# Performance work log

Measured on AMD Instinct MI355X. Metric: run time of the kernel, lower is better.

Reference implementation:

```python
import jax, jax.numpy as jnp
import numpy as np

N, E, C = 50000, 600000, 128
BN_EPS = 1e-5
NORM_EPS = 1e-12


def _edgeconv(x, src, dst, wa, ba, g, be, rm, rv, wb, bb):
    # PyG EdgeConv: message = MLP(concat(x_i, x_j - x_i)); aggr='add' at target i
    x_i = x[dst]                      # [E, C] target features
    x_j = x[src]                      # [E, C] source features
    m = jnp.concatenate([x_i, x_j - x_i], axis=-1)   # [E, 2C]
    m = jax.nn.relu(m @ wa.T + ba)                   # Linear(2C->C) + ReLU
    m = (m - rm) * (g * jax.lax.rsqrt(rv + BN_EPS)) + be  # BatchNorm1d (eval)
    m = m @ wb.T + bb                                # Linear(C->C)
    return jax.ops.segment_sum(m, dst, num_segments=x.shape[0])  # [N, C]


def _lin(k, fan_in, shape):
    bound = 1.0 / np.sqrt(fan_in)
    return jax.random.uniform(k, shape, jnp.float32, -bound, bound)


def setup_inputs() -> dict:
    key = jax.random.key(0)
    ks = jax.random.split(key, 16)
    inp = {
        "x": jax.random.normal(ks[0], (N, C), jnp.float32),
        "edge_index": jax.random.randint(ks[1], (2, E), 0, N, jnp.int64),
    }
    # layer 1 params
    inp["w1a"] = _lin(ks[2], 2 * C, (C, 2 * C)); inp["b1a"] = _lin(ks[3], 2 * C, (C,))
    inp["g1"] = jnp.ones((C,), jnp.float32) + 0.1 * jax.random.normal(ks[4], (C,))
    inp["be1"] = 0.1 * jax.random.normal(ks[5], (C,))
    inp["rm1"] = 0.1 * jax.random.normal(ks[6], (C,))
    inp["rv1"] = 0.5 + jax.random.uniform(ks[7], (C,))
    inp["w1b"] = _lin(ks[8], C, (C, C)); inp["b1b"] = _lin(ks[9], C, (C,))
    # layer 2 params
    inp["w2a"] = _lin(ks[10], 2 * C, (C, 2 * C)); inp["b2a"] = _lin(ks[11], 2 * C, (C,))
    inp["g2"] = jnp.ones((C,), jnp.float32) + 0.1 * jax.random.normal(ks[12], (C,))
    inp["be2"] = 0.1 * jax.random.normal(ks[13], (C,))
    inp["rm2"] = 0.1 * jax.random.normal(ks[14], (C,))
    inp["rv2"] = 0.5 + jax.random.uniform(ks[15], (C,))
    k2 = jax.random.split(ks[15], 2)
    inp["w2b"] = _lin(k2[0], C, (C, C)); inp["b2b"] = _lin(k2[1], C, (C,))
    return inp


def reference(x, edge_index, w1a, b1a, g1, be1, rm1, rv1, w1b, b1b,
              w2a, b2a, g2, be2, rm2, rv2, w2b, b2b):
    src, dst = edge_index[0], edge_index[1]
    # layer 1 (all but last): conv -> relu -> L2 normalize -> dropout(eval=identity)
    h = _edgeconv(x, src, dst, w1a, b1a, g1, be1, rm1, rv1, w1b, b1b)
    h = jax.nn.relu(h)
    h = h / jnp.maximum(jnp.linalg.norm(h, axis=-1, keepdims=True), NORM_EPS)
    # last layer: conv only
    return _edgeconv(h, src, dst, w2a, b2a, g2, be2, rm2, rv2, w2b, b2b)
```

## Files before the change

kernel.cpp:

```cpp
#include <hip/hip_runtime.h>

#define CCH 128
#define WPAD 136
typedef unsigned short ushort;
typedef __attribute__((ext_vector_type(8))) short bf16x8_t;
typedef __attribute__((ext_vector_type(4))) float f32x4;

union ABu { bf16x8_t v; ushort u[8]; uint4 q; };

__device__ __forceinline__ ushort f2b(float f) {
  union { float f; unsigned u; } v{f};
  unsigned r = v.u + 0x7fffu + ((v.u >> 16) & 1u);
  return (ushort)(r >> 16);
}
__device__ __forceinline__ float b2f(ushort s) {
  union { unsigned u; float f; } v{(unsigned)s << 16};
  return v.f;
}

__global__ __launch_bounds__(256) void k_pre(const float* __restrict__ w1a,
                                             const float* __restrict__ w1b,
                                             const float* __restrict__ w2a,
                                             const float* __restrict__ w2b,
                                             ushort* __restrict__ Wcat1, ushort* __restrict__ Wb1,
                                             ushort* __restrict__ Wcat2, ushort* __restrict__ Wb2,
                                             const void* __restrict__ ei, int* __restrict__ deg,
                                             int E) {
  const int b = blockIdx.x, t = threadIdx.x;
  if (b < 128) {
    int i = b * 256 + t;
    int c = i >> 7, k = i & 127;
    float v = (c < 128) ? w1a[c * 256 + k] - w1a[c * 256 + 128 + k]
                        : w1a[(c - 128) * 256 + 128 + k];
    Wcat1[i] = f2b(v);
    if (i < 16384) Wb1[i] = f2b(w1b[i]);
  } else if (b < 256) {
    int i = (b - 128) * 256 + t;
    int c = i >> 7, k = i & 127;
    float v = (c < 128) ? w2a[c * 256 + k] - w2a[c * 256 + 128 + k]
                        : w2a[(c - 128) * 256 + 128 + k];
    Wcat2[i] = f2b(v);
    if (i < 16384) Wb2[i] = f2b(w2b[i]);
  } else {
    __shared__ int nz;
    if (t == 0) nz = 0;
    __syncthreads();
    int e = (b - 256) * 256 + t;
    unsigned hi = (e < E) ? ((const unsigned*)ei)[2 * (size_t)e + 1] : 0u;
    if (hi) atomicAdd(&nz, 1);
    __syncthreads();
    bool i64 = (nz == 0);
    if (e < E) {
      int d = i64 ? (int)((const long long*)ei)[(size_t)E + e]
                  : ((const int*)ei)[(size_t)E + e];
      atomicAdd(&deg[d], 1);
    }
  }
}

__global__ __launch_bounds__(256) void k_rowptr(const int* __restrict__ deg,
                                                const int* __restrict__ bsum,
                                                int* __restrict__ rowptr,
                                                int n, int nb, int Etot) {
  __shared__ int s[256];
  const int t = threadIdx.x, b = blockIdx.x;
  s[t] = (t < nb && t < b) ? bsum[t] : 0;
  __syncthreads();
  for (int off = 128; off > 0; off >>= 1) {
    if (t < off) s[t] += s[t + off];
    __syncthreads();
  }
  int boffset = s[0];
  __syncthreads();
  int i = b * 256 + t;
  int v = (i < n) ? deg[i] : 0;
  s[t] = v; __syncthreads();
  for (int off = 1; off < 256; off <<= 1) {
    int tv = (t >= off) ? s[t - off] : 0;
    __syncthreads();
    s[t] += tv;
    __syncthreads();
  }
  if (i < n) rowptr[i] = boffset + s[t] - v;
  if (b == gridDim.x - 1 && t == 0) rowptr[n] = Etot;
}

__global__ __launch_bounds__(256) void k_scatter(const void* __restrict__ ei,
                                                 const int* __restrict__ rowptr,
                                                 int* __restrict__ cnt,
                                                 int* __restrict__ esrc, int E) {
  __shared__ int nz;
  const int t = threadIdx.x;
  if (t == 0) nz = 0;
  __syncthreads();
  int e = blockIdx.x * 256 + t;
  unsigned hi = (e < E) ? ((const unsigned*)ei)[2 * (size_t)e + 1] : 0u;
  if (hi) atomicAdd(&nz, 1);
  __syncthreads();
  bool i64 = (nz == 0);
  if (e < E) {
    int d, sv;
    if (i64) {
      sv = (int)((const long long*)ei)[(size_t)e];
      d  = (int)((const long long*)ei)[(size_t)E + e];
    } else {
      sv = ((const int*)ei)[(size_t)e];
      d  = ((const int*)ei)[(size_t)E + e];
    }
    int pos = rowptr[d] + atomicAdd(&cnt[d], 1);
    esrc[pos] = sv;
  }
}

__device__ __forceinline__ void stage_w(const ushort* __restrict__ Wp,
                                        ushort* __restrict__ wlds, int t) {
  for (int i = t; i < 128 * 16; i += 256) {
    int row = i >> 4, ch = i & 15;
    *(uint4*)&wlds[row * WPAD + ch * 8] = *(const uint4*)&Wp[row * CCH + ch * 8];
  }
}

__device__ __forceinline__ void load_a1_bf16(const ushort* __restrict__ XB,
                                             int ar, int quad, int nN, ABu a[4]) {
#pragma unroll
  for (int kk = 0; kk < 4; ++kk)
    a[kk].q = (ar < nN) ? *(const uint4*)(XB + (size_t)ar * CCH + kk * 32 + quad * 8)
                        : make_uint4(0, 0, 0, 0);
}

__device__ __forceinline__ void load_a1_f32(const float* __restrict__ X,
                                            int ar, int quad, int nN, ABu a[4]) {
#pragma unroll
  for (int kk = 0; kk < 4; ++kk) {
    if (ar < nN) {
      const float* p = X + (size_t)ar * CCH + kk * 32 + quad * 8;
      float4 f0 = *(const float4*)p, f1 = *(const float4*)(p + 4);
      a[kk].u[0] = f2b(f0.x); a[kk].u[1] = f2b(f0.y);
      a[kk].u[2] = f2b(f0.z); a[kk].u[3] = f2b(f0.w);
      a[kk].u[4] = f2b(f1.x); a[kk].u[5] = f2b(f1.y);
      a[kk].u[6] = f2b(f1.z); a[kk].u[7] = f2b(f1.w);
    } else a[kk].q = make_uint4(0, 0, 0, 0);
  }
}

__device__ __forceinline__ void load_a1_lds(const ushort* __restrict__ hlds,
                                            int lr, int quad, ABu a[4]) {
#pragma unroll
  for (int kk = 0; kk < 4; ++kk)
    a[kk].q = *(const uint4*)&hlds[lr * WPAD + kk * 32 + quad * 8];
}

__device__ __forceinline__ void mma1(const ABu a[4],
                                     const ushort* __restrict__ wlds,
                                     int ln, int quad, f32x4 acc[8]) {
#pragma unroll
  for (int s = 0; s < 8; ++s) acc[s] = (f32x4){0.f, 0.f, 0.f, 0.f};
#pragma unroll
  for (int s = 0; s < 8; ++s) {
#pragma unroll
    for (int kk = 0; kk < 4; ++kk) {
      ABu b;
      b.q = *(const uint4*)&wlds[(s * 16 + ln) * WPAD + kk * 32 + quad * 8];
      acc[s] = __builtin_amdgcn_mfma_f32_16x16x32_bf16(a[kk].v, b.v, acc[s], 0, 0, 0);
    }
  }
}

__device__ __forceinline__ void epi1(f32x4 acc[8], int rowb, int ln, int quad, int nN,
                                     const float* bias, int half, ushort* dst) {
#pragma unroll
  for (int s = 0; s < 8; ++s) {
    int col = s * 16 + ln;
    float bv = half ? 0.f : bias[col];
#pragma unroll
    for (int r = 0; r < 4; ++r) {
      int row = rowb + quad * 4 + r;
      if (row < nN) dst[(size_t)row * CCH + col] = f2b(acc[s][r] + bv);
    }
  }
}

__global__ __launch_bounds__(256) void k_mix1(const float* __restrict__ x,
                                              const ushort* __restrict__ Wcat,
                                              const float* __restrict__ bias,
                                              ushort* __restrict__ A1,
                                              ushort* __restrict__ A2, int nN,
                                              const int* __restrict__ deg,
                                              int* __restrict__ bsum, int gG, int n) {
  __shared__ ushort wlds[128 * WPAD];
  const int t = threadIdx.x;
  if ((int)blockIdx.x >= gG) {
    int* s = (int*)wlds;
    int bb = blockIdx.x - gG;
    int i = bb * 256 + t;
    s[t] = (i < n) ? deg[i] : 0;
    __syncthreads();
    for (int off = 128; off > 0; off >>= 1) {
      if (t < off) s[t] += s[t + off];
      __syncthreads();
    }
    if (t == 0) bsum[bb] = s[0];
    return;
  }
  const int wave = t >> 6, lane = t & 63;
  const int ln = lane & 15, quad = lane >> 4;
  const int rowb = blockIdx.x * 64 + wave * 16;
  stage_w(Wcat, wlds, t);
  ABu a[4];
  load_a1_f32(x, rowb + ln, quad, nN, a);
  __syncthreads();
  f32x4 acc[8];
  mma1(a, wlds, ln, quad, acc);
  epi1(acc, rowb, ln, quad, nN, bias, 0, A1);
  __syncthreads();
  stage_w(Wcat + 128 * CCH, wlds, t);
  __syncthreads();
  mma1(a, wlds, ln, quad, acc);
  epi1(acc, rowb, ln, quad, nN, bias, 1, A2);
}

__global__ __launch_bounds__(256) void k_fuse12(const ushort* __restrict__ MB,
                                                const ushort* __restrict__ Wb1,
                                                const float* __restrict__ b1b,
                                                const ushort* __restrict__ Wcat2,
                                                const float* __restrict__ b2a,
                                                const int* __restrict__ deg,
                                                ushort* __restrict__ B0,
                                                ushort* __restrict__ B1, int nN) {
  __shared__ ushort wlds[128 * WPAD];
  __shared__ ushort hlds[64 * WPAD];
  const int t = threadIdx.x, wave = t >> 6, lane = t & 63;
  const int ln = lane & 15, quad = lane >> 4;
  const int rowb = blockIdx.x * 64 + wave * 16;
  const int lrb = wave * 16;

  stage_w(Wb1, wlds, t);
  ABu a[4];
  load_a1_bf16(MB, rowb + ln, quad, nN, a);
  int dg[4];
#pragma unroll
  for (int r = 0; r < 4; ++r) {
    int row = rowb + quad * 4 + r;
    dg[r] = (row < nN) ? deg[row] : 0;
  }
  __syncthreads();
  f32x4 acc[8];
  mma1(a, wlds, ln, quad, acc);

  float biasv[8];
#pragma unroll
  for (int s = 0; s < 8; ++s) biasv[s] = b1b[s * 16 + ln];
#pragma unroll
  for (int r = 0; r < 4; ++r) {
    int row = rowb + quad * 4 + r;
    int lrow = lrb + quad * 4 + r;
    float dn = (float)dg[r];
    float vals[8];
    float ss = 0.f;
#pragma unroll
    for (int s = 0; s < 8; ++s) {
      float v = fmaxf(acc[s][r] + dn * biasv[s], 0.f);
      vals[s] = v;
      ss += v * v;
    }
    ss += __shfl_xor(ss, 1, 64);
    ss += __shfl_xor(ss, 2, 64);
    ss += __shfl_xor(ss, 4, 64);
    ss += __shfl_xor(ss, 8, 64);
    float inv = 1.0f / fmaxf(sqrtf(ss), 1e-12f);
#pragma unroll
    for (int s = 0; s < 8; ++s)
      hlds[lrow * WPAD + s * 16 + ln] = (row < nN) ? f2b(vals[s] * inv) : (ushort)0;
  }
  __syncthreads();

  stage_w(Wcat2, wlds, t);
  load_a1_lds(hlds, lrb + ln, quad, a);
  __syncthreads();
  mma1(a, wlds, ln, quad, acc);
  epi1(acc, rowb, ln, quad, nN, b2a, 0, B0);
  __syncthreads();

  stage_w(Wcat2 + 128 * CCH, wlds, t);
  __syncthreads();
  mma1(a, wlds, ln, quad, acc);
  epi1(acc, rowb, ln, quad, nN, b2a, 1, B1);
}

__global__ __launch_bounds__(256) void k_gemmf(const ushort* __restrict__ XB,
                                               const ushort* __restrict__ W,
                                               const float* __restrict__ bias,
                                               const int* __restrict__ deg,
                                               float* __restrict__ OUT, int nN) {
  __shared__ ushort wlds[128 * WPAD];
  const int t = threadIdx.x;
  stage_w(W, wlds, t);
  const int wave = t >> 6, lane = t & 63;
  const int ln = lane & 15, quad = lane >> 4;
  const int rowb = blockIdx.x * 64 + wave * 16;
  ABu a[4];
  load_a1_bf16(XB, rowb + ln, quad, nN, a);
  int dg[4];
#pragma unroll
  for (int r = 0; r < 4; ++r) {
    int row = rowb + quad * 4 + r;
    dg[r] = (row < nN) ? deg[row] : 0;
  }
  __syncthreads();
  f32x4 acc[8];
  mma1(a, wlds, ln, quad, acc);
  float biasv[8];
#pragma unroll
  for (int s = 0; s < 8; ++s) biasv[s] = bias[s * 16 + ln];
#pragma unroll
  for (int r = 0; r < 4; ++r) {
    int row = rowb + quad * 4 + r;
    if (row >= nN) continue;
    float dn = (float)dg[r];
#pragma unroll
    for (int s = 0; s < 8; ++s)
      OUT[(size_t)row * CCH + s * 16 + ln] = acc[s][r] + dn * biasv[s];
  }
}

__global__ __launch_bounds__(256) void k_aggr(const ushort* __restrict__ A1,
                                              const ushort* __restrict__ A2,
                                              const int* __restrict__ rowptr,
                                              const int* __restrict__ esrc,
                                              const float* __restrict__ g,
                                              const float* __restrict__ be,
                                              const float* __restrict__ rm,
                                              const float* __restrict__ rv,
                                              ushort* __restrict__ M, int nNodes) {
  int node = blockIdx.x * 4 + (threadIdx.x >> 6);
  if (node >= nNodes) return;
  int lane = threadIdx.x & 63;
  int q = lane >> 4;
  int c = (lane & 15) * 8;

  uint4 aq = *(const uint4*)&A1[(size_t)node * CCH + c];
  float a[8] = {b2f((ushort)aq.x), b2f((ushort)(aq.x >> 16)),
                b2f((ushort)aq.y), b2f((ushort)(aq.y >> 16)),
                b2f((ushort)aq.z), b2f((ushort)(aq.z >> 16)),
                b2f((ushort)aq.w), b2f((ushort)(aq.w >> 16))};
  int r0 = rowptr[node], r1 = rowptr[node + 1];
  float s[8] = {0.f, 0.f, 0.f, 0.f, 0.f, 0.f, 0.f, 0.f};

  auto acc8 = [&](uint4 w) {
    const unsigned* p = (const unsigned*)&w;
#pragma unroll
    for (int j = 0; j < 4; ++j) {
      s[2*j]   += fmaxf(a[2*j]   + b2f((ushort)p[j]), 0.f);
      s[2*j+1] += fmaxf(a[2*j+1] + b2f((ushort)(p[j] >> 16)), 0.f);
    }
  };

  for (int base = r0; base < r1; base += 64) {
    int navail = r1 - base; if (navail > 64) navail = 64;
    int myi = (lane < navail) ? esrc[base + lane] : 0;
    int g4 = navail >> 2, tail = navail & 3;
    int j = 0;
    for (; j + 4 <= g4; j += 4) {
      int p0 = j * 4 + q;
      int i0 = __shfl(myi, p0, 64);
      int i1 = __shfl(myi, p0 + 4, 64);
      int i2 = __shfl(myi, p0 + 8, 64);
      int i3 = __shfl(myi, p0 + 12, 64);
      uint4 w0 = *(const uint4*)&A2[(size_t)i0 * CCH + c];
      uint4 w1 = *(const uint4*)&A2[(size_t)i1 * CCH + c];
      uint4 w2 = *(const uint4*)&A2[(size_t)i2 * CCH + c];
      uint4 w3 = *(const uint4*)&A2[(size_t)i3 * CCH + c];
      acc8(w0); acc8(w1); acc8(w2); acc8(w3);
    }
    for (; j < g4; ++j) {
      int i0 = __shfl(myi, j * 4 + q, 64);
      acc8(*(const uint4*)&A2[(size_t)i0 * CCH + c]);
    }
    int pt = g4 * 4 + q; if (pt > 63) pt = 63;
    int it = __shfl(myi, pt, 64);
    if (q < tail) acc8(*(const uint4*)&A2[(size_t)it * CCH + c]);
  }
#pragma unroll
  for (int j = 0; j < 8; ++j) {
    s[j] += __shfl_xor(s[j], 16, 64);
    s[j] += __shfl_xor(s[j], 32, 64);
  }

  if (q == 0) {
    float dn = (float)(r1 - r0);
    unsigned p[4];
#pragma unroll
    for (int j = 0; j < 4; ++j) {
      float sc0 = g[c + 2*j]     * rsqrtf(rv[c + 2*j]     + 1e-5f);
      float sc1 = g[c + 2*j + 1] * rsqrtf(rv[c + 2*j + 1] + 1e-5f);
      float o0 = sc0 * s[2*j]     + dn * (be[c + 2*j]     - rm[c + 2*j]     * sc0);
      float o1 = sc1 * s[2*j + 1] + dn * (be[c + 2*j + 1] - rm[c + 2*j + 1] * sc1);
      p[j] = (unsigned)f2b(o0) | ((unsigned)f2b(o1) << 16);
    }
    *(uint4*)&M[(size_t)node * CCH + c] = make_uint4(p[0], p[1], p[2], p[3]);
  }
}

extern "C" void kernel_launch(void* const* d_in, const int* in_sizes, int n_in,
                              void* d_out, int out_size, void* d_ws, size_t ws_size,
                              hipStream_t stream) {
  const float* x   = (const float*)d_in[0];
  const void*  ei  = d_in[1];
  const float* w1a = (const float*)d_in[2];
  const float* b1a = (const float*)d_in[3];
  const float* g1  = (const float*)d_in[4];
  const float* be1 = (const float*)d_in[5];
  const float* rm1 = (const float*)d_in[6];
  const float* rv1 = (const float*)d_in[7];
  const float* w1b = (const float*)d_in[8];
  const float* b1b = (const float*)d_in[9];
  const float* w2a = (const float*)d_in[10];
  const float* b2a = (const float*)d_in[11];
  const float* g2  = (const float*)d_in[12];
  const float* be2 = (const float*)d_in[13];
  const float* rm2 = (const float*)d_in[14];
  const float* rv2 = (const float*)d_in[15];
  const float* w2b = (const float*)d_in[16];
  const float* b2b = (const float*)d_in[17];

  const int N = in_sizes[0] / CCH;
  const int E = in_sizes[1] / 2;
  const size_t NC = (size_t)N * CCH;

  int* deg    = (int*)d_ws;
  int* cnt    = deg + N;
  int* rowptr = cnt + N;
  int* bsum   = rowptr + N + 1;
  int* esrc   = bsum + 256;
  uintptr_t pw = ((uintptr_t)(esrc + E) + 63) & ~(uintptr_t)63;
  ushort* Wcat1 = (ushort*)pw;
  ushort* Wcat2 = Wcat1 + 32768;
  ushort* Wb1   = Wcat2 + 32768;
  ushort* Wb2   = Wb1 + 16384;
  uintptr_t pb = ((uintptr_t)(Wb2 + 16384) + 63) & ~(uintptr_t)63;
  ushort* B0 = (ushort*)pb;
  ushort* B1 = B0 + NC;
  ushort* MB = B1 + NC;

  const int gE  = (E + 255) / 256;
  const int gS  = (N + 255) / 256;
  const int gG  = (N + 63) / 64;
  const int gA  = (N + 3) / 4;

  hipMemsetAsync(deg, 0, sizeof(int) * 2 * (size_t)N, stream);
  k_pre<<<256 + gE, 256, 0, stream>>>(w1a, w1b, w2a, w2b,
                                      Wcat1, Wb1, Wcat2, Wb2, ei, deg, E);
  k_mix1<<<gG + gS, 256, 0, stream>>>(x, Wcat1, b1a, B0, B1, N, deg, bsum, gG, N);
  k_rowptr<<<gS, 256, 0, stream>>>(deg, bsum, rowptr, N, gS, E);
  k_scatter<<<gE, 256, 0, stream>>>(ei, rowptr, cnt, esrc, E);

  k_aggr<<<gA, 256, 0, stream>>>(B0, B1, rowptr, esrc, g1, be1, rm1, rv1, MB, N);
  k_fuse12<<<gG, 256, 0, stream>>>(MB, Wb1, b1b, Wcat2, b2a, deg, B0, B1, N);
  k_aggr<<<gA, 256, 0, stream>>>(B0, B1, rowptr, esrc, g2, be2, rm2, rv2, MB, N);
  k_gemmf<<<gG, 256, 0, stream>>>(MB, Wb2, b2b, deg, (float*)d_out, N);
}
```

Measured before the change: 299.2 us.

## Fuse edge aggregation into the following GEMM kernels via LDS staging

```diff
diff --git a/kernel.cpp b/kernel.cpp
--- a/kernel.cpp
+++ b/kernel.cpp
@@ -120,14 +120,6 @@
   }
 }
 
-__device__ __forceinline__ void load_a1_bf16(const ushort* __restrict__ XB,
-                                             int ar, int quad, int nN, ABu a[4]) {
-#pragma unroll
-  for (int kk = 0; kk < 4; ++kk)
-    a[kk].q = (ar < nN) ? *(const uint4*)(XB + (size_t)ar * CCH + kk * 32 + quad * 8)
-                        : make_uint4(0, 0, 0, 0);
-}
-
 __device__ __forceinline__ void load_a1_f32(const float* __restrict__ X,
                                             int ar, int quad, int nN, ABu a[4]) {
 #pragma unroll
@@ -176,6 +168,85 @@
     for (int r = 0; r < 4; ++r) {
       int row = rowb + quad * 4 + r;
       if (row < nN) dst[(size_t)row * CCH + col] = f2b(acc[s][r] + bv);
+    }
+  }
+}
+
+__device__ __forceinline__ void aggr16(const ushort* __restrict__ A1,
+                                       const ushort* __restrict__ A2,
+                                       const int* __restrict__ rowptr,
+                                       const int* __restrict__ esrc,
+                                       const float* __restrict__ g,
+                                       const float* __restrict__ be,
+                                       const float* __restrict__ rm,
+                                       const float* __restrict__ rv,
+                                       ushort* __restrict__ mw,
+                                       float* __restrict__ dw,
+                                       int nodeb, int lane, int nN) {
+  const int q = lane >> 4;
+  const int c = (lane & 15) * 8;
+  float sc[8], off[8];
+#pragma unroll
+  for (int j = 0; j < 8; ++j) {
+    float s0 = g[c + j] * rsqrtf(rv[c + j] + 1e-5f);
+    sc[j] = s0; off[j] = be[c + j] - rm[c + j] * s0;
+  }
+  for (int i = 0; i < 16; ++i) {
+    int node = nodeb + i;
+    float s[8] = {0.f, 0.f, 0.f, 0.f, 0.f, 0.f, 0.f, 0.f};
+    float dn = 0.f;
+    if (node < nN) {
+      uint4 aq = *(const uint4*)&A1[(size_t)node * CCH + c];
+      float af[8] = {b2f((ushort)aq.x), b2f((ushort)(aq.x >> 16)),
+                     b2f((ushort)aq.y), b2f((ushort)(aq.y >> 16)),
+                     b2f((ushort)aq.z), b2f((ushort)(aq.z >> 16)),
+                     b2f((ushort)aq.w), b2f((ushort)(aq.w >> 16))};
+      int r0 = rowptr[node], r1 = rowptr[node + 1];
+      dn = (float)(r1 - r0);
+      for (int base = r0; base < r1; base += 64) {
+        int navail = r1 - base; if (navail > 64) navail = 64;
+        int myi = (lane < navail) ? esrc[base + lane] : 0;
+        int nr = (navail + 3) >> 2;
+        for (int j0 = 0; j0 < nr; j0 += 4) {
+          uint4 w[4];
+          int pe[4];
+#pragma unroll
+          for (int u = 0; u < 4; ++u) {
+            int p = (j0 + u) * 4 + q;
+            pe[u] = p;
+            int pc = (p < navail) ? p : (navail - 1);
+            int idx = __shfl(myi, pc, 64);
+            w[u] = *(const uint4*)&A2[(size_t)idx * CCH + c];
+          }
+#pragma unroll
+          for (int u = 0; u < 4; ++u) {
+            if (pe[u] < navail) {
+              const unsigned* p = (const unsigned*)&w[u];
+#pragma unroll
+              for (int j = 0; j < 4; ++j) {
+                s[2*j]   += fmaxf(af[2*j]   + b2f((ushort)p[j]), 0.f);
+                s[2*j+1] += fmaxf(af[2*j+1] + b2f((ushort)(p[j] >> 16)), 0.f);
+              }
+            }
+          }
+        }
+      }
+#pragma unroll
+      for (int j = 0; j < 8; ++j) {
+        s[j] += __shfl_xor(s[j], 16, 64);
+        s[j] += __shfl_xor(s[j], 32, 64);
+      }
+    }
+    if (lane == 0) dw[i] = dn;
+    if (q == 0) {
+      unsigned pk[4];
+#pragma unroll
+      for (int j = 0; j < 4; ++j) {
+        float o0 = sc[2*j]   * s[2*j]   + dn * off[2*j];
+        float o1 = sc[2*j+1] * s[2*j+1] + dn * off[2*j+1];
+        pk[j] = (unsigned)f2b(o0) | ((unsigned)f2b(o1) << 16);
+      }
+      *(uint4*)&mw[i * WPAD + c] = make_uint4(pk[0], pk[1], pk[2], pk[3]);
     }
   }
 }
@@ -219,30 +290,34 @@
   epi1(acc, rowb, ln, quad, nN, bias, 1, A2);
 }
 
-__global__ __launch_bounds__(256) void k_fuse12(const ushort* __restrict__ MB,
-                                                const ushort* __restrict__ Wb1,
-                                                const float* __restrict__ b1b,
-                                                const ushort* __restrict__ Wcat2,
-                                                const float* __restrict__ b2a,
-                                                const int* __restrict__ deg,
-                                                ushort* __restrict__ B0,
-                                                ushort* __restrict__ B1, int nN) {
+__global__ __launch_bounds__(256) void k_af1(const ushort* __restrict__ A1,
+                                             const ushort* __restrict__ A2,
+                                             const int* __restrict__ rowptr,
+                                             const int* __restrict__ esrc,
+                                             const float* __restrict__ g,
+                                             const float* __restrict__ be,
+                                             const float* __restrict__ rm,
+                                             const float* __restrict__ rv,
+                                             const ushort* __restrict__ Wb1,
+                                             const float* __restrict__ b1b,
+                                             const ushort* __restrict__ Wcat2,
+                                             const float* __restrict__ b2a,
+                                             ushort* __restrict__ C0,
+                                             ushort* __restrict__ C1, int nN) {
   __shared__ ushort wlds[128 * WPAD];
-  __shared__ ushort hlds[64 * WPAD];
+  __shared__ ushort mlds[64 * WPAD];
+  __shared__ float dlds[64];
   const int t = threadIdx.x, wave = t >> 6, lane = t & 63;
   const int ln = lane & 15, quad = lane >> 4;
-  const int rowb = blockIdx.x * 64 + wave * 16;
   const int lrb = wave * 16;
+  const int rowb = blockIdx.x * 64 + lrb;
 
   stage_w(Wb1, wlds, t);
+  aggr16(A1, A2, rowptr, esrc, g, be, rm, rv,
+         &mlds[lrb * WPAD], &dlds[lrb], rowb, lane, nN);
+
   ABu a[4];
-  load_a1_bf16(MB, rowb + ln, quad, nN, a);
-  int dg[4];
-#pragma unroll
-  for (int r = 0; r < 4; ++r) {
-    int row = rowb + quad * 4 + r;
-    dg[r] = (row < nN) ? deg[row] : 0;
-  }
+  load_a1_lds(mlds, lrb + ln, quad, a);
   __syncthreads();
   f32x4 acc[8];
   mma1(a, wlds, ln, quad, acc);
@@ -254,7 +329,7 @@
   for (int r = 0; r < 4; ++r) {
     int row = rowb + quad * 4 + r;
     int lrow = lrb + quad * 4 + r;
-    float dn = (float)dg[r];
+    float dn = dlds[lrow];
     float vals[8];
     float ss = 0.f;
 #pragma unroll
@@ -270,134 +345,63 @@
     float inv = 1.0f / fmaxf(sqrtf(ss), 1e-12f);
 #pragma unroll
     for (int s = 0; s < 8; ++s)
-      hlds[lrow * WPAD + s * 16 + ln] = (row < nN) ? f2b(vals[s] * inv) : (ushort)0;
-  }
+      mlds[lrow * WPAD + s * 16 + ln] = (row < nN) ? f2b(vals[s] * inv) : (ushort)0;
+  }
+  ABu a2[4];
+  load_a1_lds(mlds, lrb + ln, quad, a2);
   __syncthreads();
 
   stage_w(Wcat2, wlds, t);
-  load_a1_lds(hlds, lrb + ln, quad, a);
-  __syncthreads();
-  mma1(a, wlds, ln, quad, acc);
-  epi1(acc, rowb, ln, quad, nN, b2a, 0, B0);
-  __syncthreads();
-
+  __syncthreads();
+  mma1(a2, wlds, ln, quad, acc);
+  epi1(acc, rowb, ln, quad, nN, b2a, 0, C0);
+  __syncthreads();
   stage_w(Wcat2 + 128 * CCH, wlds, t);
   __syncthreads();
-  mma1(a, wlds, ln, quad, acc);
-  epi1(acc, rowb, ln, quad, nN, b2a, 1, B1);
-}
-
-__global__ __launch_bounds__(256) void k_gemmf(const ushort* __restrict__ XB,
-                                               const ushort* __restrict__ W,
-                                               const float* __restrict__ bias,
-                                               const int* __restrict__ deg,
-                                               float* __restrict__ OUT, int nN) {
+  mma1(a2, wlds, ln, quad, acc);
+  epi1(acc, rowb, ln, quad, nN, b2a, 1, C1);
+}
+
+__global__ __launch_bounds__(256) void k_af2(const ushort* __restrict__ A1,
+                                             const ushort* __restrict__ A2,
+                                             const int* __restrict__ rowptr,
+                                             const int* __restrict__ esrc,
+                                             const float* __restrict__ g,
+                                             const float* __restrict__ be,
+                                             const float* __restrict__ rm,
+                                             const float* __restrict__ rv,
+                                             const ushort* __restrict__ Wb2,
+                                             const float* __restrict__ b2b,
+                                             float* __restrict__ OUT, int nN) {
   __shared__ ushort wlds[128 * WPAD];
-  const int t = threadIdx.x;
-  stage_w(W, wlds, t);
-  const int wave = t >> 6, lane = t & 63;
+  __shared__ ushort mlds[64 * WPAD];
+  __shared__ float dlds[64];
+  const int t = threadIdx.x, wave = t >> 6, lane = t & 63;
   const int ln = lane & 15, quad = lane >> 4;
-  const int rowb = blockIdx.x * 64 + wave * 16;
+  const int lrb = wave * 16;
+  const int rowb = blockIdx.x * 64 + lrb;
+
+  stage_w(Wb2, wlds, t);
+  aggr16(A1, A2, rowptr, esrc, g, be, rm, rv,
+         &mlds[lrb * WPAD], &dlds[lrb], rowb, lane, nN);
+
   ABu a[4];
-  load_a1_bf16(XB, rowb + ln, quad, nN, a);
-  int dg[4];
-#pragma unroll
-  for (int r = 0; r < 4; ++r) {
-    int row = rowb + quad * 4 + r;
-    dg[r] = (row < nN) ? deg[row] : 0;
-  }
+  load_a1_lds(mlds, lrb + ln, quad, a);
   __syncthreads();
   f32x4 acc[8];
   mma1(a, wlds, ln, quad, acc);
+
   float biasv[8];
 #pragma unroll
-  for (int s = 0; s < 8; ++s) biasv[s] = bias[s * 16 + ln];
+  for (int s = 0; s < 8; ++s) biasv[s] = b2b[s * 16 + ln];
 #pragma unroll
   for (int r = 0; r < 4; ++r) {
     int row = rowb + quad * 4 + r;
     if (row >= nN) continue;
-    float dn = (float)dg[r];
+    float dn = dlds[lrb + quad * 4 + r];
 #pragma unroll
     for (int s = 0; s < 8; ++s)
       OUT[(size_t)row * CCH + s * 16 + ln] = acc[s][r] + dn * biasv[s];
-  }
-}
-
-__global__ __launch_bounds__(256) void k_aggr(const ushort* __restrict__ A1,
-                                              const ushort* __restrict__ A2,
-                                              const int* __restrict__ rowptr,
-                                              const int* __restrict__ esrc,
-                                              const float* __restrict__ g,
-                                              const float* __restrict__ be,
-                                              const float* __restrict__ rm,
-                                              const float* __restrict__ rv,
-                                              ushort* __restrict__ M, int nNodes) {
-  int node = blockIdx.x * 4 + (threadIdx.x >> 6);
-  if (node >= nNodes) return;
-  int lane = threadIdx.x & 63;
-  int q = lane >> 4;
-  int c = (lane & 15) * 8;
-
-  uint4 aq = *(const uint4*)&A1[(size_t)node * CCH + c];
-  float a[8] = {b2f((ushort)aq.x), b2f((ushort)(aq.x >> 16)),
-                b2f((ushort)aq.y), b2f((ushort)(aq.y >> 16)),
-                b2f((ushort)aq.z), b2f((ushort)(aq.z >> 16)),
-                b2f((ushort)aq.w), b2f((ushort)(aq.w >> 16))};
-  int r0 = rowptr[node], r1 = rowptr[node + 1];
-  float s[8] = {0.f, 0.f, 0.f, 0.f, 0.f, 0.f, 0.f, 0.f};
-
-  auto acc8 = [&](uint4 w) {
-    const unsigned* p = (const unsigned*)&w;
-#pragma unroll
-    for (int j = 0; j < 4; ++j) {
-      s[2*j]   += fmaxf(a[2*j]   + b2f((ushort)p[j]), 0.f);
-      s[2*j+1] += fmaxf(a[2*j+1] + b2f((ushort)(p[j] >> 16)), 0.f);
-    }
-  };
-
-  for (int base = r0; base < r1; base += 64) {
-    int navail = r1 - base; if (navail > 64) navail = 64;
-    int myi = (lane < navail) ? esrc[base + lane] : 0;
-    int g4 = navail >> 2, tail = navail & 3;
-    int j = 0;
-    for (; j + 4 <= g4; j += 4) {
-      int p0 = j * 4 + q;
-      int i0 = __shfl(myi, p0, 64);
-      int i1 = __shfl(myi, p0 + 4, 64);
-      int i2 = __shfl(myi, p0 + 8, 64);
-      int i3 = __shfl(myi, p0 + 12, 64);
-      uint4 w0 = *(const uint4*)&A2[(size_t)i0 * CCH + c];
-      uint4 w1 = *(const uint4*)&A2[(size_t)i1 * CCH + c];
-      uint4 w2 = *(const uint4*)&A2[(size_t)i2 * CCH + c];
-      uint4 w3 = *(const uint4*)&A2[(size_t)i3 * CCH + c];
-      acc8(w0); acc8(w1); acc8(w2); acc8(w3);
-    }
-    for (; j < g4; ++j) {
-      int i0 = __shfl(myi, j * 4 + q, 64);
-      acc8(*(const uint4*)&A2[(size_t)i0 * CCH + c]);
-    }
-    int pt = g4 * 4 + q; if (pt > 63) pt = 63;
-    int it = __shfl(myi, pt, 64);
-    if (q < tail) acc8(*(const uint4*)&A2[(size_t)it * CCH + c]);
-  }
-#pragma unroll
-  for (int j = 0; j < 8; ++j) {
-    s[j] += __shfl_xor(s[j], 16, 64);
-    s[j] += __shfl_xor(s[j], 32, 64);
-  }
-
-  if (q == 0) {
-    float dn = (float)(r1 - r0);
-    unsigned p[4];
-#pragma unroll
-    for (int j = 0; j < 4; ++j) {
-      float sc0 = g[c + 2*j]     * rsqrtf(rv[c + 2*j]     + 1e-5f);
-      float sc1 = g[c + 2*j + 1] * rsqrtf(rv[c + 2*j + 1] + 1e-5f);
-      float o0 = sc0 * s[2*j]     + dn * (be[c + 2*j]     - rm[c + 2*j]     * sc0);
-      float o1 = sc1 * s[2*j + 1] + dn * (be[c + 2*j + 1] - rm[c + 2*j + 1] * sc1);
-      p[j] = (unsigned)f2b(o0) | ((unsigned)f2b(o1) << 16);
-    }
-    *(uint4*)&M[(size_t)node * CCH + c] = make_uint4(p[0], p[1], p[2], p[3]);
   }
 }
 
@@ -441,21 +445,21 @@
   ushort* B0 = (ushort*)pb;
   ushort* B1 = B0 + NC;
   ushort* MB = B1 + NC;
+  ushort* HB = MB + NC;
 
   const int gE  = (E + 255) / 256;
   const int gS  = (N + 255) / 256;
-  const int gG  = (N + 63) / 64;
-  const int gA  = (N + 3) / 4;
+  const int gG2 = (N + 63) / 64;
 
   hipMemsetAsync(deg, 0, sizeof(int) * 2 * (size_t)N, stream);
   k_pre<<<256 + gE, 256, 0, stream>>>(w1a, w1b, w2a, w2b,
                                       Wcat1, Wb1, Wcat2, Wb2, ei, deg, E);
-  k_mix1<<<gG + gS, 256, 0, stream>>>(x, Wcat1, b1a, B0, B1, N, deg, bsum, gG, N);
+  k_mix1<<<gG2 + gS, 256, 0, stream>>>(x, Wcat1, b1a, B0, B1, N, deg, bsum, gG2, N);
   k_rowptr<<<gS, 256, 0, stream>>>(deg, bsum, rowptr, N, gS, E);
   k_scatter<<<gE, 256, 0, stream>>>(ei, rowptr, cnt, esrc, E);
 
-  k_aggr<<<gA, 256, 0, stream>>>(B0, B1, rowptr, esrc, g1, be1, rm1, rv1, MB, N);
-  k_fuse12<<<gG, 256, 0, stream>>>(MB, Wb1, b1b, Wcat2, b2a, deg, B0, B1, N);
-  k_aggr<<<gA, 256, 0, stream>>>(B0, B1, rowptr, esrc, g2, be2, rm2, rv2, MB, N);
-  k_gemmf<<<gG, 256, 0, stream>>>(MB, Wb2, b2b, deg, (float*)d_out, N);
-}
+  k_af1<<<gG2, 256, 0, stream>>>(B0, B1, rowptr, esrc, g1, be1, rm1, rv1,
+                                 Wb1, b1b, Wcat2, b2a, MB, HB, N);
+  k_af2<<<gG2, 256, 0, stream>>>(MB, HB, rowptr, esrc, g2, be2, rm2, rv2,
+                                 Wb2, b2b, (float*)d_out, N);
+}
```

Measured after the change: 347.2 us. +16.0%, slower.
